# Performance work log

Hardware: AMD Instinct MI355X
Metric: run time of the kernel (lower is better)

## Reference

```python
import jax, jax.numpy as jnp
import numpy as np

B, N, D, H = 4, 4096, 1024, 16
DK = D // H


def setup_inputs() -> dict:
    key = jax.random.key(0)
    ks = jax.random.split(key, 11)
    s = 0.02  # small init scale for weights
    return {
        "query": jax.random.normal(ks[0], (B, N, D), jnp.float32),
        "key": jax.random.normal(ks[1], (B, N, D), jnp.float32),
        "value": jax.random.normal(ks[2], (B, N, D), jnp.float32),
        "Wq": jax.random.normal(ks[3], (D, D), jnp.float32) * s,
        "bq": jax.random.normal(ks[4], (D,), jnp.float32) * s,
        "Wk": jax.random.normal(ks[5], (D, D), jnp.float32) * s,
        "bk": jax.random.normal(ks[6], (D,), jnp.float32) * s,
        "Wv": jax.random.normal(ks[7], (D, D), jnp.float32) * s,
        "bv": jax.random.normal(ks[8], (D,), jnp.float32) * s,
        "Wo": jax.random.normal(ks[9], (D, D), jnp.float32) * s,
        "bo": jax.random.normal(ks[10], (D,), jnp.float32) * s,
    }


def reference(query, key, value, Wq, bq, Wk, bk, Wv, bv, Wo, bo):
    b, n, d = query.shape
    h, dk = H, d // H

    def proj(x, W, bias):
        # torch Linear: y = x @ W.T + b ; then split heads -> [b,h,n,dk]
        y = x @ W.T + bias
        return y.reshape(b, n, h, dk).transpose(0, 2, 1, 3)

    q = proj(query, Wq, bq)
    k = proj(key, Wk, bk)
    v = proj(value, Wv, bv)

    # linear attention (Efficient Attention, arXiv:1812.01243)
    q = jax.nn.softmax(q, axis=-1) * (1.0 / np.sqrt(dk).astype(np.float32))
    k = jax.nn.softmax(k, axis=-2)  # softmax over sequence dim
    ctx = jnp.einsum('bhnd,bhne->bhde', k, v)   # [b,h,dk,dk]
    out = jnp.einsum('bhnd,bhde->bhne', q, ctx)  # [b,h,n,dk]

    out = out.transpose(0, 2, 1, 3).reshape(b, n, d)
    return out @ Wo.T + bo
```

## Files before the change

kernel.cpp:

```cpp
#include <hip/hip_runtime.h>
#include <hip/hip_bf16.h>

#define B_ 4
#define N_ 4096
#define D_ 1024
#define H_ 16

typedef __attribute__((ext_vector_type(4))) float f32x4;
typedef __attribute__((ext_vector_type(8))) short s16x8;
typedef __attribute__((ext_vector_type(4))) unsigned int u32x4;

__device__ __forceinline__ ushort f2bf(float f) {
  union { float f; unsigned u; } v; v.f = f;
  unsigned u = v.u;
  return (ushort)((u + 0x7fffu + ((u >> 16) & 1u)) >> 16);
}

__device__ __forceinline__ void gld16(const ushort* g, ushort* lds_base) {
  __builtin_amdgcn_global_load_lds(
      (const __attribute__((address_space(1))) unsigned int*)g,
      (__attribute__((address_space(3))) unsigned int*)lds_base, 16, 0, 0);
}

__device__ __forceinline__ unsigned cvtpk(float lo, float hi) {
  unsigned r;
  asm("v_cvt_pk_bf16_f32 %0, %1, %2" : "=v"(r) : "v"(lo), "v"(hi));
  return r;
}

__global__ void conv_w_kernel(const float* __restrict__ w0, const float* __restrict__ w1,
                              const float* __restrict__ w2, const float* __restrict__ w3,
                              ushort* __restrict__ dst) {
  const int z = blockIdx.z;
  const float* src = z == 0 ? w0 : z == 1 ? w1 : z == 2 ? w2 : w3;
  ushort* d = dst + (long)z * (D_ * D_);
  const long i0 = ((long)blockIdx.x * 256 + threadIdx.x) * 8;
  const long STR = (long)128 * 256 * 8;
#pragma unroll
  for (int u = 0; u < 4; ++u) {
    f32x4 a = *(const f32x4*)(src + i0 + u * STR);
    f32x4 b = *(const f32x4*)(src + i0 + u * STR + 4);
    s16x8 o;
    o[0] = (short)f2bf(a[0]); o[1] = (short)f2bf(a[1]); o[2] = (short)f2bf(a[2]); o[3] = (short)f2bf(a[3]);
    o[4] = (short)f2bf(b[0]); o[5] = (short)f2bf(b[1]); o[6] = (short)f2bf(b[2]); o[7] = (short)f2bf(b[3]);
    *(s16x8*)(d + i0 + u * STR) = o;
  }
}

template <int EPI, bool AFP32>
__global__ __launch_bounds__(256, 2) void gemm_bt_kernel(
    const void* __restrict__ Av, const ushort* __restrict__ Bm,
    void* __restrict__ Cv, const float* __restrict__ bias, float* __restrict__ kpart,
    int K, long sA, long sB, long sC) {
  __shared__ ushort As[128 * 32];
  __shared__ ushort Bs[128 * 32];
  const int z = blockIdx.z;
  Bm += (long)z * sB;
  const int m0 = blockIdx.x * 128, n0 = blockIdx.y * 128;
  const int N = 1024;
  const int tid = threadIdx.x;
  const int wave = tid >> 6, lane = tid & 63;
  const int fl = lane & 15, fh = lane >> 4;
  const int wm = wave >> 1, wn = wave & 1;
  f32x4 acc[4][4] = {};
  const int rb0 = tid >> 2, kb0 = (tid & 3) * 8;
  const int rb1 = (tid + 256) >> 2, kb1 = ((tid + 256) & 3) * 8;
  ushort* ldsB0 = Bs + wave * 512;
  ushort* ldsB1 = Bs + 2048 + wave * 512;
  ushort* ldsA0 = As + wave * 512;
  ushort* ldsA1 = As + 2048 + wave * 512;

  const float* Af = (const float*)Av;
  const ushort* Ab = (const ushort*)Av + (long)z * sA;

  const int ar = tid >> 2, ac = tid & 3;
  const float* ap0 = AFP32 ? (Af + (long)(m0 + ar) * K + ac * 8) : nullptr;
  const float* ap1 = AFP32 ? (ap0 + (long)64 * K) : nullptr;
  ushort* wp0 = As + ar * 32 + ac * 8;
  ushort* wp1 = As + (ar + 64) * 32 + ac * 8;
  f32x4 pa0, pa1, pa2, pa3;
  if constexpr (AFP32) {
    pa0 = *(const f32x4*)(ap0);
    pa1 = *(const f32x4*)(ap0 + 4);
    pa2 = *(const f32x4*)(ap1);
    pa3 = *(const f32x4*)(ap1 + 4);
  }

  for (int kk = 0; kk < K; kk += 32) {
    __syncthreads();
    gld16(Bm + (long)(n0 + rb0) * K + kk + kb0, ldsB0);
    gld16(Bm + (long)(n0 + rb1) * K + kk + kb1, ldsB1);
    if constexpr (AFP32) {
      u32x4 w0, w1;
      w0[0] = cvtpk(pa0[0], pa0[1]); w0[1] = cvtpk(pa0[2], pa0[3]);
      w0[2] = cvtpk(pa1[0], pa1[1]); w0[3] = cvtpk(pa1[2], pa1[3]);
      w1[0] = cvtpk(pa2[0], pa2[1]); w1[1] = cvtpk(pa2[2], pa2[3]);
      w1[2] = cvtpk(pa3[0], pa3[1]); w1[3] = cvtpk(pa3[2], pa3[3]);
      *(u32x4*)wp0 = w0;
      *(u32x4*)wp1 = w1;
      if (kk + 32 < K) {
        pa0 = *(const f32x4*)(ap0 + kk + 32);
        pa1 = *(const f32x4*)(ap0 + kk + 36);
        pa2 = *(const f32x4*)(ap1 + kk + 32);
        pa3 = *(const f32x4*)(ap1 + kk + 36);
      }
    } else {
      gld16(Ab + (long)(m0 + rb0) * K + kk + kb0, ldsA0);
      gld16(Ab + (long)(m0 + rb1) * K + kk + kb1, ldsA1);
    }
    __syncthreads();
    s16x8 fa[4], fb[4];
#pragma unroll
    for (int i = 0; i < 4; ++i)
      fa[i] = *(const s16x8*)(As + (wm * 64 + i * 16 + fl) * 32 + fh * 8);
#pragma unroll
    for (int j = 0; j < 4; ++j)
      fb[j] = *(const s16x8*)(Bs + (wn * 64 + j * 16 + fl) * 32 + fh * 8);
#pragma unroll
    for (int i = 0; i < 4; ++i)
#pragma unroll
      for (int j = 0; j < 4; ++j)
        acc[i][j] = __builtin_amdgcn_mfma_f32_16x16x32_bf16(fa[i], fb[j], acc[i][j], 0, 0, 0);
  }

  if constexpr (EPI == 0) {
    ushort* C = (ushort*)Cv;
#pragma unroll
    for (int j = 0; j < 4; ++j) {
      int col = n0 + wn * 64 + j * 16 + fl;
#pragma unroll
      for (int i = 0; i < 4; ++i)
#pragma unroll
        for (int r = 0; r < 4; ++r) {
          int row = m0 + wm * 64 + i * 16 + fh * 4 + r;
          C[(long)row * N + col] = f2bf(acc[i][j][r]);
        }
    }
  } else if constexpr (EPI == 1) {
    ushort* C = (ushort*)Cv;
    float bcol[4];
#pragma unroll
    for (int j = 0; j < 4; ++j) bcol[j] = bias[n0 + wn * 64 + j * 16 + fl];
#pragma unroll
    for (int i = 0; i < 4; ++i)
#pragma unroll
      for (int r = 0; r < 4; ++r) {
        float v[4];
#pragma unroll
        for (int j = 0; j < 4; ++j) v[j] = acc[i][j][r] + bcol[j];
        float m = fmaxf(fmaxf(v[0], v[1]), fmaxf(v[2], v[3]));
#pragma unroll
        for (int o = 1; o <= 8; o <<= 1) m = fmaxf(m, __shfl_xor(m, o));
        float e[4], s = 0.f;
#pragma unroll
        for (int j = 0; j < 4; ++j) { e[j] = __expf(v[j] - m); s += e[j]; }
#pragma unroll
        for (int o = 1; o <= 8; o <<= 1) s += __shfl_xor(s, o);
        float sc = 0.125f / s;
        int row = m0 + wm * 64 + i * 16 + fh * 4 + r;
#pragma unroll
        for (int j = 0; j < 4; ++j)
          C[(long)row * N + n0 + wn * 64 + j * 16 + fl] = f2bf(e[j] * sc);
      }
  } else if constexpr (EPI == 2) {
    ushort* C = (ushort*)Cv;
    float csum[4] = {};
#pragma unroll
    for (int j = 0; j < 4; ++j) {
      int col = n0 + wn * 64 + j * 16 + fl;
#pragma unroll
      for (int i = 0; i < 4; ++i)
#pragma unroll
        for (int r = 0; r < 4; ++r) {
          int row = m0 + wm * 64 + i * 16 + fh * 4 + r;
          float e = __expf(acc[i][j][r]);
          csum[j] += e;
          C[(long)row * N + col] = f2bf(e);
        }
    }
#pragma unroll
    for (int j = 0; j < 4; ++j) {
#pragma unroll
      for (int o = 16; o <= 32; o <<= 1) csum[j] += __shfl_xor(csum[j], o);
    }
    if (fh == 0) {
      int b = m0 >> 12;
      int chunk = ((m0 & 4095) >> 7) * 2 + wm;
#pragma unroll
      for (int j = 0; j < 4; ++j)
        kpart[(long)b * 65536 + (long)chunk * 1024 + n0 + wn * 64 + j * 16 + fl] = csum[j];
    }
  } else {
    float* C = (float*)Cv + (long)z * sC;
#pragma unroll
    for (int j = 0; j < 4; ++j) {
      int col = n0 + wn * 64 + j * 16 + fl;
      float bv = bias[col];
#pragma unroll
      for (int i = 0; i < 4; ++i)
#pragma unroll
        for (int r = 0; r < 4; ++r) {
          int row = m0 + wm * 64 + i * 16 + fh * 4 + r;
          C[(long)row * N + col] = acc[i][j][r] + bv;
        }
    }
  }
}

__global__ void ksm2_kernel(const float* __restrict__ kpart, float* __restrict__ colinv) {
  int idx = blockIdx.x * 256 + threadIdx.x;
  int b = idx >> 10, d = idx & 1023;
  float s = 0.f;
  for (int c = 0; c < 64; ++c) s += kpart[(long)b * 65536 + (long)c * 1024 + d];
  colinv[idx] = 1.0f / s;
}

__global__ __launch_bounds__(256, 2) void ctx_partial_kernel(
    const ushort* __restrict__ Ksm, const ushort* __restrict__ Vp, float* __restrict__ part) {
  __shared__ ushort Ks[128 * 64];
  __shared__ ushort Vs[128 * 64];
  const int chunk = blockIdx.x;
  const int bh = blockIdx.y;
  const int b = bh >> 4, h = bh & 15;
  const int tid = threadIdx.x, wave = tid >> 6, lane = tid & 63;
  const int fl = lane & 15, fh = lane >> 4;
  f32x4 acc[4] = {};
  for (int t = 0; t < 4; ++t) {
    const long base = ((long)(b * N_ + chunk * 512 + t * 128)) * D_ + h * 64;
    __syncthreads();
#pragma unroll
    for (int i = 0; i < 4; ++i) {
      int c = i * 256 + tid;
      int r = c >> 3, k8 = (c & 7) * 8;
      ushort* lk = Ks + (long)(i * 256 + wave * 64) * 8;
      ushort* lv = Vs + (long)(i * 256 + wave * 64) * 8;
      gld16(Ksm + base + (long)r * D_ + k8, lk);
      gld16(Vp + base + (long)r * D_ + k8, lv);
    }
    __syncthreads();
#pragma unroll
    for (int s = 0; s < 4; ++s) {
      s16x8 fa;
#pragma unroll
      for (int j = 0; j < 8; ++j)
        fa[j] = (short)Ks[(s * 32 + fh * 8 + j) * 64 + wave * 16 + fl];
#pragma unroll
      for (int jt = 0; jt < 4; ++jt) {
        s16x8 fb;
#pragma unroll
        for (int j = 0; j < 8; ++j)
          fb[j] = (short)Vs[(s * 32 + fh * 8 + j) * 64 + jt * 16 + fl];
        acc[jt] = __builtin_amdgcn_mfma_f32_16x16x32_bf16(fa, fb, acc[jt], 0, 0, 0);
      }
    }
  }
  float* dst = part + ((long)chunk * 64 + bh) * 4096;
#pragma unroll
  for (int jt = 0; jt < 4; ++jt)
#pragma unroll
    for (int r = 0; r < 4; ++r)
      dst[(wave * 16 + fh * 4 + r) * 64 + jt * 16 + fl] = acc[jt][r];
}

__global__ void ctx_reduce_kernel(const float* __restrict__ part, const float* __restrict__ bv,
                                  const float* __restrict__ colinv, ushort* __restrict__ ctxb) {
  int idx = blockIdx.x * 256 + threadIdx.x;
  int e = idx & 63;
  int dk = (idx >> 6) & 63;
  int h = (idx >> 12) & 15;
  int b = idx >> 16;
  float s = 0.f;
#pragma unroll
  for (int c = 0; c < 8; ++c) s += part[(long)c * 262144 + idx];
  ctxb[idx] = f2bf(s * colinv[b * 1024 + h * 64 + dk] + bv[h * 64 + e]);
}

__global__ __launch_bounds__(256, 2) void mb_kernel(
    const ushort* __restrict__ Wob, const ushort* __restrict__ ctxb, ushort* __restrict__ Mb) {
  const int o0 = blockIdx.x * 64, h = blockIdx.y, b = blockIdx.z;
  const int tid = threadIdx.x, wave = tid >> 6, lane = tid & 63;
  const int fl = lane & 15, fh = lane >> 4;
  const ushort* ctxh = ctxb + ((long)(b * 16 + h)) * 4096;
  f32x4 acc[4] = {};
#pragma unroll
  for (int s = 0; s < 2; ++s) {
    s16x8 fa = *(const s16x8*)(Wob + (long)(o0 + wave * 16 + fl) * D_ + h * 64 + s * 32 + fh * 8);
#pragma unroll
    for (int jt = 0; jt < 4; ++jt) {
      s16x8 fb = *(const s16x8*)(ctxh + (long)(jt * 16 + fl) * 64 + s * 32 + fh * 8);
      acc[jt] = __builtin_amdgcn_mfma_f32_16x16x32_bf16(fa, fb, acc[jt], 0, 0, 0);
    }
  }
  ushort* dst = Mb + (long)b * (D_ * D_);
#pragma unroll
  for (int jt = 0; jt < 4; ++jt)
#pragma unroll
    for (int r = 0; r < 4; ++r)
      dst[(long)(o0 + wave * 16 + fh * 4 + r) * D_ + h * 64 + jt * 16 + fl] = f2bf(acc[jt][r]);
}

extern "C" void kernel_launch(void* const* d_in, const int* in_sizes, int n_in,
                              void* d_out, int out_size, void* d_ws, size_t ws_size,
                              hipStream_t stream) {
  const float* q_in = (const float*)d_in[0];
  const float* k_in = (const float*)d_in[1];
  const float* v_in = (const float*)d_in[2];
  const float* Wq = (const float*)d_in[3];
  const float* bq = (const float*)d_in[4];
  const float* Wk = (const float*)d_in[5];
  const float* Wv = (const float*)d_in[7];
  const float* bv = (const float*)d_in[8];
  const float* Wo = (const float*)d_in[9];
  const float* bo = (const float*)d_in[10];

  char* ws = (char*)d_ws;
  ushort* Wb = (ushort*)(ws + 0);
  ushort* Qp = (ushort*)(ws + 8388608);
  ushort* Kp = (ushort*)(ws + 41943040);
  ushort* Vp = (ushort*)(ws + 75497472);
  float* kpart = (float*)(ws + 109051904);
  float* colinv = (float*)(ws + 110100480);
  float* ctxpart = (float*)(ws + 110116864);
  ushort* ctxb = (ushort*)(ws + 118505472);
  ushort* Mb = (ushort*)(ws + 119029760);

  ushort* Wbq = Wb;
  ushort* Wbk = Wb + 1048576;
  ushort* Wbv = Wb + 2097152;
  ushort* Wbo = Wb + 3145728;

  conv_w_kernel<<<dim3(128, 1, 4), 256, 0, stream>>>(Wq, Wk, Wv, Wo, Wb);

  gemm_bt_kernel<1, true><<<dim3(128, 8, 1), 256, 0, stream>>>(
      q_in, Wbq, Qp, bq, nullptr, 1024, 0, 0, 0);
  gemm_bt_kernel<2, true><<<dim3(128, 8, 1), 256, 0, stream>>>(
      k_in, Wbk, Kp, nullptr, kpart, 1024, 0, 0, 0);
  gemm_bt_kernel<0, true><<<dim3(128, 8, 1), 256, 0, stream>>>(
      v_in, Wbv, Vp, nullptr, nullptr, 1024, 0, 0, 0);

  ksm2_kernel<<<16, 256, 0, stream>>>(kpart, colinv);

  ctx_partial_kernel<<<dim3(8, 64), 256, 0, stream>>>(Kp, Vp, ctxpart);
  ctx_reduce_kernel<<<1024, 256, 0, stream>>>(ctxpart, bv, colinv, ctxb);
  mb_kernel<<<dim3(16, 16, 4), 256, 0, stream>>>(Wbo, ctxb, Mb);

  gemm_bt_kernel<3, false><<<dim3(32, 8, 4), 256, 0, stream>>>(
      Qp, Mb, (float*)d_out, bo, nullptr, 1024,
      (long)4096 * 1024, (long)1024 * 1024, (long)4096 * 1024);
}
```

Baseline: 270.7 us.

## Pipeline GEMM with 4-stage LDS ring, 8 waves and swizzled shared layout

Rewrites the projection/output GEMM main loop into a multi-stage software pipeline: a 4-deep LDS ring buffer with async global-to-LDS loads issued several k-steps ahead, explicit vmcnt waits and single barriers per step. Blocks grow to 512 threads (8 waves, each owning a 32x64 sub-tile), and the LDS layout is XOR-swizzled to avoid bank conflicts on fragment reads. The fp32 A operand is prefetched two steps ahead in registers and converted to bf16. Key partial sums double in count because of the new wave layout, so the workspace offsets and the reduction loop are adjusted. This hardcodes K=1024 and adds complex manual wait-count logic that is easy to get wrong.

```diff
diff --git a/kernel.cpp b/kernel.cpp
--- a/kernel.cpp
+++ b/kernel.cpp
@@ -27,6 +27,11 @@
   asm("v_cvt_pk_bf16_f32 %0, %1, %2" : "=v"(r) : "v"(lo), "v"(hi));
   return r;
 }
+
+#define WAITVM(N) asm volatile("s_waitcnt vmcnt(" #N ")" ::: "memory")
+#define LGKM0 asm volatile("s_waitcnt lgkmcnt(0)" ::: "memory")
+#define SBAR __builtin_amdgcn_sched_barrier(0)
+#define BARRIER __builtin_amdgcn_s_barrier()
 
 __global__ void conv_w_kernel(const float* __restrict__ w0, const float* __restrict__ w1,
                               const float* __restrict__ w2, const float* __restrict__ w3,
@@ -48,12 +53,12 @@
 }
 
 template <int EPI, bool AFP32>
-__global__ __launch_bounds__(256, 2) void gemm_bt_kernel(
+__global__ __launch_bounds__(512, 4) void gemm_bt_kernel(
     const void* __restrict__ Av, const ushort* __restrict__ Bm,
     void* __restrict__ Cv, const float* __restrict__ bias, float* __restrict__ kpart,
-    int K, long sA, long sB, long sC) {
-  __shared__ ushort As[128 * 32];
-  __shared__ ushort Bs[128 * 32];
+    long sA, long sB, long sC) {
+  __shared__ ushort As[16384];
+  __shared__ ushort Bs[16384];
   const int z = blockIdx.z;
   Bm += (long)z * sB;
   const int m0 = blockIdx.x * 128, n0 = blockIdx.y * 128;
@@ -62,66 +67,99 @@
   const int wave = tid >> 6, lane = tid & 63;
   const int fl = lane & 15, fh = lane >> 4;
   const int wm = wave >> 1, wn = wave & 1;
-  f32x4 acc[4][4] = {};
-  const int rb0 = tid >> 2, kb0 = (tid & 3) * 8;
-  const int rb1 = (tid + 256) >> 2, kb1 = ((tid + 256) & 3) * 8;
-  ushort* ldsB0 = Bs + wave * 512;
-  ushort* ldsB1 = Bs + 2048 + wave * 512;
-  ushort* ldsA0 = As + wave * 512;
-  ushort* ldsA1 = As + 2048 + wave * 512;
-
-  const float* Af = (const float*)Av;
-  const ushort* Ab = (const ushort*)Av + (long)z * sA;
-
+  f32x4 acc[2][4] = {};
+
+  const int rB = tid >> 2;
+  const int sgB = ((tid & 3) ^ ((tid >> 3) & 3)) * 8;
+  const ushort* Bp0 = Bm + (long)(n0 + rB) * 1024 + sgB;
+  ushort* BsD0 = Bs + tid * 8;
+  const ushort* Ab = AFP32 ? nullptr : ((const ushort*)Av + (long)z * sA);
+  const ushort* Ap0 = AFP32 ? nullptr : (Ab + (long)(m0 + rB) * 1024 + sgB);
+  ushort* AsD0 = As + tid * 8;
   const int ar = tid >> 2, ac = tid & 3;
-  const float* ap0 = AFP32 ? (Af + (long)(m0 + ar) * K + ac * 8) : nullptr;
-  const float* ap1 = AFP32 ? (ap0 + (long)64 * K) : nullptr;
-  ushort* wp0 = As + ar * 32 + ac * 8;
-  ushort* wp1 = As + (ar + 64) * 32 + ac * 8;
-  f32x4 pa0, pa1, pa2, pa3;
+  const float* apA = AFP32 ? ((const float*)Av + (long)(m0 + ar) * 1024 + ac * 8) : nullptr;
+  const int awoff = ar * 32 + ((ac ^ ((tid >> 3) & 3)) * 8);
+  const int fro = fl * 32 + ((fh ^ ((fl >> 1) & 3)) * 8);
+
+  f32x4 pE0, pE1, pO0, pO1;
+
+#define ISSUE_B(T) do { gld16(Bp0 + (T) * 32, BsD0 + (((T) & 3) << 12)); } while (0)
+#define ISSUE_A16(T) do { gld16(Ap0 + (T) * 32, AsD0 + (((T) & 3) << 12)); } while (0)
+#define ISSUE_AF(T, P) do { \
+    P##0 = *(const f32x4*)(apA + (T) * 32); \
+    P##1 = *(const f32x4*)(apA + (T) * 32 + 4); } while (0)
+#define CVT_WRITE(T, P) do { \
+    u32x4 _w; \
+    _w[0] = cvtpk(P##0[0], P##0[1]); _w[1] = cvtpk(P##0[2], P##0[3]); \
+    _w[2] = cvtpk(P##1[0], P##1[1]); _w[3] = cvtpk(P##1[2], P##1[3]); \
+    *(u32x4*)(As + (((T) & 3) << 12) + awoff) = _w; } while (0)
+#define MFMA_STEP(T) do { \
+    const ushort* _a = As + (((T) & 3) << 12); \
+    const ushort* _b = Bs + (((T) & 3) << 12); \
+    s16x8 fa[2], fb[4]; \
+    _Pragma("unroll") for (int i = 0; i < 2; ++i) \
+      fa[i] = *(const s16x8*)(_a + (wm * 32 + i * 16) * 32 + fro); \
+    _Pragma("unroll") for (int j = 0; j < 4; ++j) \
+      fb[j] = *(const s16x8*)(_b + (wn * 64 + j * 16) * 32 + fro); \
+    _Pragma("unroll") for (int i = 0; i < 2; ++i) \
+      _Pragma("unroll") for (int j = 0; j < 4; ++j) \
+        acc[i][j] = __builtin_amdgcn_mfma_f32_16x16x32_bf16(fa[i], fb[j], acc[i][j], 0, 0, 0); \
+    } while (0)
+
   if constexpr (AFP32) {
-    pa0 = *(const f32x4*)(ap0);
-    pa1 = *(const f32x4*)(ap0 + 4);
-    pa2 = *(const f32x4*)(ap1);
-    pa3 = *(const f32x4*)(ap1 + 4);
-  }
-
-  for (int kk = 0; kk < K; kk += 32) {
-    __syncthreads();
-    gld16(Bm + (long)(n0 + rb0) * K + kk + kb0, ldsB0);
-    gld16(Bm + (long)(n0 + rb1) * K + kk + kb1, ldsB1);
-    if constexpr (AFP32) {
-      u32x4 w0, w1;
-      w0[0] = cvtpk(pa0[0], pa0[1]); w0[1] = cvtpk(pa0[2], pa0[3]);
-      w0[2] = cvtpk(pa1[0], pa1[1]); w0[3] = cvtpk(pa1[2], pa1[3]);
-      w1[0] = cvtpk(pa2[0], pa2[1]); w1[1] = cvtpk(pa2[2], pa2[3]);
-      w1[2] = cvtpk(pa3[0], pa3[1]); w1[3] = cvtpk(pa3[2], pa3[3]);
-      *(u32x4*)wp0 = w0;
-      *(u32x4*)wp1 = w1;
-      if (kk + 32 < K) {
-        pa0 = *(const f32x4*)(ap0 + kk + 32);
-        pa1 = *(const f32x4*)(ap0 + kk + 36);
-        pa2 = *(const f32x4*)(ap1 + kk + 32);
-        pa3 = *(const f32x4*)(ap1 + kk + 36);
-      }
-    } else {
-      gld16(Ab + (long)(m0 + rb0) * K + kk + kb0, ldsA0);
-      gld16(Ab + (long)(m0 + rb1) * K + kk + kb1, ldsA1);
-    }
-    __syncthreads();
-    s16x8 fa[4], fb[4];
-#pragma unroll
-    for (int i = 0; i < 4; ++i)
-      fa[i] = *(const s16x8*)(As + (wm * 64 + i * 16 + fl) * 32 + fh * 8);
-#pragma unroll
-    for (int j = 0; j < 4; ++j)
-      fb[j] = *(const s16x8*)(Bs + (wn * 64 + j * 16 + fl) * 32 + fh * 8);
-#pragma unroll
-    for (int i = 0; i < 4; ++i)
-#pragma unroll
-      for (int j = 0; j < 4; ++j)
-        acc[i][j] = __builtin_amdgcn_mfma_f32_16x16x32_bf16(fa[i], fb[j], acc[i][j], 0, 0, 0);
-  }
+    ISSUE_B(0); SBAR;
+    ISSUE_AF(0, pE); SBAR;
+    ISSUE_B(1); SBAR;
+    ISSUE_AF(1, pO); SBAR;
+    ISSUE_B(2); SBAR;
+    CVT_WRITE(0, pE);
+#pragma unroll 1
+    for (int t = 0; t < 28; t += 2) {
+      WAITVM(6); LGKM0; BARRIER; SBAR;
+      ISSUE_AF(t + 2, pE); SBAR;
+      ISSUE_B(t + 3); SBAR;
+      CVT_WRITE(t + 1, pO);
+      MFMA_STEP(t);
+      WAITVM(6); LGKM0; BARRIER; SBAR;
+      ISSUE_AF(t + 3, pO); SBAR;
+      ISSUE_B(t + 4); SBAR;
+      CVT_WRITE(t + 2, pE);
+      MFMA_STEP(t + 1);
+    }
+    WAITVM(6); LGKM0; BARRIER; SBAR;
+    ISSUE_AF(30, pE); SBAR;
+    ISSUE_B(31); SBAR;
+    CVT_WRITE(29, pO);
+    MFMA_STEP(28);
+    WAITVM(6); LGKM0; BARRIER; SBAR;
+    ISSUE_AF(31, pO); SBAR;
+    CVT_WRITE(30, pE);
+    MFMA_STEP(29);
+    WAITVM(5); LGKM0; BARRIER; SBAR;
+    CVT_WRITE(31, pO);
+    MFMA_STEP(30);
+    WAITVM(2); LGKM0; BARRIER; SBAR;
+    MFMA_STEP(31);
+  } else {
+    ISSUE_A16(0); SBAR; ISSUE_B(0); SBAR;
+    ISSUE_A16(1); SBAR; ISSUE_B(1); SBAR;
+    ISSUE_A16(2); SBAR; ISSUE_B(2); SBAR;
+#pragma unroll 1
+    for (int t = 0; t < 29; ++t) {
+      WAITVM(4); BARRIER; SBAR;
+      ISSUE_A16(t + 3); SBAR;
+      ISSUE_B(t + 3); SBAR;
+      MFMA_STEP(t);
+    }
+    WAITVM(4); BARRIER; SBAR; MFMA_STEP(29);
+    WAITVM(2); BARRIER; SBAR; MFMA_STEP(30);
+    WAITVM(0); BARRIER; SBAR; MFMA_STEP(31);
+  }
+#undef ISSUE_B
+#undef ISSUE_A16
+#undef ISSUE_AF
+#undef CVT_WRITE
+#undef MFMA_STEP
 
   if constexpr (EPI == 0) {
     ushort* C = (ushort*)Cv;
@@ -129,10 +167,10 @@
     for (int j = 0; j < 4; ++j) {
       int col = n0 + wn * 64 + j * 16 + fl;
 #pragma unroll
-      for (int i = 0; i < 4; ++i)
+      for (int i = 0; i < 2; ++i)
 #pragma unroll
         for (int r = 0; r < 4; ++r) {
-          int row = m0 + wm * 64 + i * 16 + fh * 4 + r;
+          int row = m0 + wm * 32 + i * 16 + fh * 4 + r;
           C[(long)row * N + col] = f2bf(acc[i][j][r]);
         }
     }
@@ -142,7 +180,7 @@
 #pragma unroll
     for (int j = 0; j < 4; ++j) bcol[j] = bias[n0 + wn * 64 + j * 16 + fl];
 #pragma unroll
-    for (int i = 0; i < 4; ++i)
+    for (int i = 0; i < 2; ++i)
 #pragma unroll
       for (int r = 0; r < 4; ++r) {
         float v[4];
@@ -157,7 +195,7 @@
 #pragma unroll
         for (int o = 1; o <= 8; o <<= 1) s += __shfl_xor(s, o);
         float sc = 0.125f / s;
-        int row = m0 + wm * 64 + i * 16 + fh * 4 + r;
+        int row = m0 + wm * 32 + i * 16 + fh * 4 + r;
 #pragma unroll
         for (int j = 0; j < 4; ++j)
           C[(long)row * N + n0 + wn * 64 + j * 16 + fl] = f2bf(e[j] * sc);
@@ -169,10 +207,10 @@
     for (int j = 0; j < 4; ++j) {
       int col = n0 + wn * 64 + j * 16 + fl;
 #pragma unroll
-      for (int i = 0; i < 4; ++i)
+      for (int i = 0; i < 2; ++i)
 #pragma unroll
         for (int r = 0; r < 4; ++r) {
-          int row = m0 + wm * 64 + i * 16 + fh * 4 + r;
+          int row = m0 + wm * 32 + i * 16 + fh * 4 + r;
           float e = __expf(acc[i][j][r]);
           csum[j] += e;
           C[(long)row * N + col] = f2bf(e);
@@ -185,10 +223,10 @@
     }
     if (fh == 0) {
       int b = m0 >> 12;
-      int chunk = ((m0 & 4095) >> 7) * 2 + wm;
+      int chunk = ((m0 & 4095) >> 7) * 4 + wm;
 #pragma unroll
       for (int j = 0; j < 4; ++j)
-        kpart[(long)b * 65536 + (long)chunk * 1024 + n0 + wn * 64 + j * 16 + fl] = csum[j];
+        kpart[(long)b * 131072 + (long)chunk * 1024 + n0 + wn * 64 + j * 16 + fl] = csum[j];
     }
   } else {
     float* C = (float*)Cv + (long)z * sC;
@@ -197,10 +235,10 @@
       int col = n0 + wn * 64 + j * 16 + fl;
       float bv = bias[col];
 #pragma unroll
-      for (int i = 0; i < 4; ++i)
+      for (int i = 0; i < 2; ++i)
 #pragma unroll
         for (int r = 0; r < 4; ++r) {
-          int row = m0 + wm * 64 + i * 16 + fh * 4 + r;
+          int row = m0 + wm * 32 + i * 16 + fh * 4 + r;
           C[(long)row * N + col] = acc[i][j][r] + bv;
         }
     }
@@ -211,7 +249,7 @@
   int idx = blockIdx.x * 256 + threadIdx.x;
   int b = idx >> 10, d = idx & 1023;
   float s = 0.f;
-  for (int c = 0; c < 64; ++c) s += kpart[(long)b * 65536 + (long)c * 1024 + d];
+  for (int c = 0; c < 128; ++c) s += kpart[(long)b * 131072 + (long)c * 1024 + d];
   colinv[idx] = 1.0f / s;
 }
 
@@ -319,10 +357,10 @@
   ushort* Kp = (ushort*)(ws + 41943040);
   ushort* Vp = (ushort*)(ws + 75497472);
   float* kpart = (float*)(ws + 109051904);
-  float* colinv = (float*)(ws + 110100480);
-  float* ctxpart = (float*)(ws + 110116864);
-  ushort* ctxb = (ushort*)(ws + 118505472);
-  ushort* Mb = (ushort*)(ws + 119029760);
+  float* colinv = (float*)(ws + 111149056);
+  float* ctxpart = (float*)(ws + 111165440);
+  ushort* ctxb = (ushort*)(ws + 119554048);
+  ushort* Mb = (ushort*)(ws + 120078336);
 
   ushort* Wbq = Wb;
   ushort* Wbk = Wb + 1048576;
@@ -331,12 +369,12 @@
 
   conv_w_kernel<<<dim3(128, 1, 4), 256, 0, stream>>>(Wq, Wk, Wv, Wo, Wb);
 
-  gemm_bt_kernel<1, true><<<dim3(128, 8, 1), 256, 0, stream>>>(
-      q_in, Wbq, Qp, bq, nullptr, 1024, 0, 0, 0);
-  gemm_bt_kernel<2, true><<<dim3(128, 8, 1), 256, 0, stream>>>(
-      k_in, Wbk, Kp, nullptr, kpart, 1024, 0, 0, 0);
-  gemm_bt_kernel<0, true><<<dim3(128, 8, 1), 256, 0, stream>>>(
-      v_in, Wbv, Vp, nullptr, nullptr, 1024, 0, 0, 0);
+  gemm_bt_kernel<1, true><<<dim3(128, 8, 1), 512, 0, stream>>>(
+      q_in, Wbq, Qp, bq, nullptr, 0, 0, 0);
+  gemm_bt_kernel<2, true><<<dim3(128, 8, 1), 512, 0, stream>>>(
+      k_in, Wbk, Kp, nullptr, kpart, 0, 0, 0);
+  gemm_bt_kernel<0, true><<<dim3(128, 8, 1), 512, 0, stream>>>(
+      v_in, Wbv, Vp, nullptr, nullptr, 0, 0, 0);
 
   ksm2_kernel<<<16, 256, 0, stream>>>(kpart, colinv);
 
@@ -344,7 +382,7 @@
   ctx_reduce_kernel<<<1024, 256, 0, stream>>>(ctxpart, bv, colinv, ctxb);
   mb_kernel<<<dim3(16, 16, 4), 256, 0, stream>>>(Wbo, ctxb, Mb);
 
-  gemm_bt_kernel<3, false><<<dim3(32, 8, 4), 256, 0, stream>>>(
-      Qp, Mb, (float*)d_out, bo, nullptr, 1024,
+  gemm_bt_kernel<3, false><<<dim3(32, 8, 4), 512, 0, stream>>>(
+      Qp, Mb, (float*)d_out, bo, nullptr,
       (long)4096 * 1024, (long)1024 * 1024, (long)4096 * 1024);
 }
```

Result: slower. 302.6 us (+11.8%).

## Merge QKV projections into one launch and XOR-swizzle LDS tiles

Applied to the files above, without the earlier changes.

Replaces the three separate projection GEMM launches with a single launch that uses blockIdx.z to pick the input, weight and epilogue. It also XOR-swizzles the LDS layout of the A and B tiles, for both the global-to-LDS loads and the fragment reads, to reduce bank conflicts. The fp32 A loading now gives each thread 16 consecutive floats of one row instead of 8 floats from two rows. The output GEMM becomes a dedicated kernel with the same swizzle. The per-z epilogue branch is uniform per block, so it adds little divergence.

```diff
diff --git a/kernel.cpp b/kernel.cpp
--- a/kernel.cpp
+++ b/kernel.cpp
@@ -47,75 +47,69 @@
   }
 }
 
-template <int EPI, bool AFP32>
-__global__ __launch_bounds__(256, 2) void gemm_bt_kernel(
-    const void* __restrict__ Av, const ushort* __restrict__ Bm,
-    void* __restrict__ Cv, const float* __restrict__ bias, float* __restrict__ kpart,
-    int K, long sA, long sB, long sC) {
-  __shared__ ushort As[128 * 32];
-  __shared__ ushort Bs[128 * 32];
+__global__ __launch_bounds__(256, 2) void gemm_qkv(
+    const float* __restrict__ q_in, const float* __restrict__ k_in,
+    const float* __restrict__ v_in, const ushort* __restrict__ Wb,
+    ushort* __restrict__ P, const float* __restrict__ bq, float* __restrict__ kpart) {
+  __shared__ ushort As[4096];
+  __shared__ ushort Bs[4096];
   const int z = blockIdx.z;
-  Bm += (long)z * sB;
+  const float* Af = z == 0 ? q_in : (z == 1 ? k_in : v_in);
+  const ushort* Bm = Wb + (long)z * 1048576;
+  ushort* C = P + (long)z * 16777216;
   const int m0 = blockIdx.x * 128, n0 = blockIdx.y * 128;
   const int N = 1024;
   const int tid = threadIdx.x;
-  const int wave = tid >> 6, lane = tid & 63;
+  const int lane = tid & 63, wave = tid >> 6;
   const int fl = lane & 15, fh = lane >> 4;
   const int wm = wave >> 1, wn = wave & 1;
   f32x4 acc[4][4] = {};
-  const int rb0 = tid >> 2, kb0 = (tid & 3) * 8;
-  const int rb1 = (tid + 256) >> 2, kb1 = ((tid + 256) & 3) * 8;
-  ushort* ldsB0 = Bs + wave * 512;
-  ushort* ldsB1 = Bs + 2048 + wave * 512;
-  ushort* ldsA0 = As + wave * 512;
-  ushort* ldsA1 = As + 2048 + wave * 512;
-
-  const float* Af = (const float*)Av;
-  const ushort* Ab = (const ushort*)Av + (long)z * sA;
-
-  const int ar = tid >> 2, ac = tid & 3;
-  const float* ap0 = AFP32 ? (Af + (long)(m0 + ar) * K + ac * 8) : nullptr;
-  const float* ap1 = AFP32 ? (ap0 + (long)64 * K) : nullptr;
-  ushort* wp0 = As + ar * 32 + ac * 8;
-  ushort* wp1 = As + (ar + 64) * 32 + ac * 8;
+
+  const int r0 = tid >> 2;
+  const int s8 = (((tid & 3) ^ ((r0 >> 1) & 3)) * 8);
+  const ushort* Bsrc0 = Bm + (long)(n0 + r0) * 1024 + s8;
+  const ushort* Bsrc1 = Bm + (long)(n0 + r0 + 64) * 1024 + s8;
+
+  const int ar = tid >> 1, ch = tid & 1;
+  const float* apA = Af + (long)(m0 + ar) * 1024 + ch * 16;
+  const int aw0 = ar * 32 + (((ch * 2) ^ ((ar >> 1) & 3)) * 8);
+  const int aw1 = ar * 32 + (((ch * 2 + 1) ^ ((ar >> 1) & 3)) * 8);
+
+  const int fro = (fh ^ ((fl >> 1) & 3)) * 8;
+
   f32x4 pa0, pa1, pa2, pa3;
-  if constexpr (AFP32) {
-    pa0 = *(const f32x4*)(ap0);
-    pa1 = *(const f32x4*)(ap0 + 4);
-    pa2 = *(const f32x4*)(ap1);
-    pa3 = *(const f32x4*)(ap1 + 4);
-  }
-
-  for (int kk = 0; kk < K; kk += 32) {
-    __syncthreads();
-    gld16(Bm + (long)(n0 + rb0) * K + kk + kb0, ldsB0);
-    gld16(Bm + (long)(n0 + rb1) * K + kk + kb1, ldsB1);
-    if constexpr (AFP32) {
+  pa0 = *(const f32x4*)(apA);
+  pa1 = *(const f32x4*)(apA + 4);
+  pa2 = *(const f32x4*)(apA + 8);
+  pa3 = *(const f32x4*)(apA + 12);
+
+  for (int kk = 0; kk < 1024; kk += 32) {
+    __syncthreads();
+    gld16(Bsrc0 + kk, Bs + tid * 8);
+    gld16(Bsrc1 + kk, Bs + 2048 + tid * 8);
+    {
       u32x4 w0, w1;
       w0[0] = cvtpk(pa0[0], pa0[1]); w0[1] = cvtpk(pa0[2], pa0[3]);
       w0[2] = cvtpk(pa1[0], pa1[1]); w0[3] = cvtpk(pa1[2], pa1[3]);
       w1[0] = cvtpk(pa2[0], pa2[1]); w1[1] = cvtpk(pa2[2], pa2[3]);
       w1[2] = cvtpk(pa3[0], pa3[1]); w1[3] = cvtpk(pa3[2], pa3[3]);
-      *(u32x4*)wp0 = w0;
-      *(u32x4*)wp1 = w1;
-      if (kk + 32 < K) {
-        pa0 = *(const f32x4*)(ap0 + kk + 32);
-        pa1 = *(const f32x4*)(ap0 + kk + 36);
-        pa2 = *(const f32x4*)(ap1 + kk + 32);
-        pa3 = *(const f32x4*)(ap1 + kk + 36);
+      *(u32x4*)(As + aw0) = w0;
+      *(u32x4*)(As + aw1) = w1;
+      if (kk + 32 < 1024) {
+        pa0 = *(const f32x4*)(apA + kk + 32);
+        pa1 = *(const f32x4*)(apA + kk + 36);
+        pa2 = *(const f32x4*)(apA + kk + 40);
+        pa3 = *(const f32x4*)(apA + kk + 44);
       }
-    } else {
-      gld16(Ab + (long)(m0 + rb0) * K + kk + kb0, ldsA0);
-      gld16(Ab + (long)(m0 + rb1) * K + kk + kb1, ldsA1);
     }
     __syncthreads();
     s16x8 fa[4], fb[4];
 #pragma unroll
     for (int i = 0; i < 4; ++i)
-      fa[i] = *(const s16x8*)(As + (wm * 64 + i * 16 + fl) * 32 + fh * 8);
+      fa[i] = *(const s16x8*)(As + (wm * 64 + i * 16 + fl) * 32 + fro);
 #pragma unroll
     for (int j = 0; j < 4; ++j)
-      fb[j] = *(const s16x8*)(Bs + (wn * 64 + j * 16 + fl) * 32 + fh * 8);
+      fb[j] = *(const s16x8*)(Bs + (wn * 64 + j * 16 + fl) * 32 + fro);
 #pragma unroll
     for (int i = 0; i < 4; ++i)
 #pragma unroll
@@ -123,24 +117,10 @@
         acc[i][j] = __builtin_amdgcn_mfma_f32_16x16x32_bf16(fa[i], fb[j], acc[i][j], 0, 0, 0);
   }
 
-  if constexpr (EPI == 0) {
-    ushort* C = (ushort*)Cv;
-#pragma unroll
-    for (int j = 0; j < 4; ++j) {
-      int col = n0 + wn * 64 + j * 16 + fl;
-#pragma unroll
-      for (int i = 0; i < 4; ++i)
-#pragma unroll
-        for (int r = 0; r < 4; ++r) {
-          int row = m0 + wm * 64 + i * 16 + fh * 4 + r;
-          C[(long)row * N + col] = f2bf(acc[i][j][r]);
-        }
-    }
-  } else if constexpr (EPI == 1) {
-    ushort* C = (ushort*)Cv;
+  if (z == 0) {
     float bcol[4];
 #pragma unroll
-    for (int j = 0; j < 4; ++j) bcol[j] = bias[n0 + wn * 64 + j * 16 + fl];
+    for (int j = 0; j < 4; ++j) bcol[j] = bq[n0 + wn * 64 + j * 16 + fl];
 #pragma unroll
     for (int i = 0; i < 4; ++i)
 #pragma unroll
@@ -162,8 +142,7 @@
         for (int j = 0; j < 4; ++j)
           C[(long)row * N + n0 + wn * 64 + j * 16 + fl] = f2bf(e[j] * sc);
       }
-  } else if constexpr (EPI == 2) {
-    ushort* C = (ushort*)Cv;
+  } else if (z == 1) {
     float csum[4] = {};
 #pragma unroll
     for (int j = 0; j < 4; ++j) {
@@ -191,19 +170,78 @@
         kpart[(long)b * 65536 + (long)chunk * 1024 + n0 + wn * 64 + j * 16 + fl] = csum[j];
     }
   } else {
-    float* C = (float*)Cv + (long)z * sC;
 #pragma unroll
     for (int j = 0; j < 4; ++j) {
       int col = n0 + wn * 64 + j * 16 + fl;
-      float bv = bias[col];
 #pragma unroll
       for (int i = 0; i < 4; ++i)
 #pragma unroll
         for (int r = 0; r < 4; ++r) {
           int row = m0 + wm * 64 + i * 16 + fh * 4 + r;
-          C[(long)row * N + col] = acc[i][j][r] + bv;
+          C[(long)row * N + col] = f2bf(acc[i][j][r]);
         }
     }
+  }
+}
+
+__global__ __launch_bounds__(256, 2) void gemm_o(const ushort* __restrict__ Ain,
+                                                 const ushort* __restrict__ Bin,
+                                                 float* __restrict__ Cout,
+                                                 const float* __restrict__ bias) {
+  __shared__ ushort As[4096];
+  __shared__ ushort Bs[4096];
+  const int z = blockIdx.z;
+  const ushort* Ab = Ain + (long)z * 4096 * 1024;
+  const ushort* Bm = Bin + (long)z * 1024 * 1024;
+  float* C = Cout + (long)z * 4096 * 1024;
+  const int m0 = blockIdx.x * 128, n0 = blockIdx.y * 128;
+  const int N = 1024;
+  const int tid = threadIdx.x;
+  const int lane = tid & 63, wave = tid >> 6;
+  const int fl = lane & 15, fh = lane >> 4;
+  const int wm = wave >> 1, wn = wave & 1;
+  f32x4 acc[4][4] = {};
+
+  const int r0 = tid >> 2;
+  const int s8 = (((tid & 3) ^ ((r0 >> 1) & 3)) * 8);
+  const ushort* Bsrc0 = Bm + (long)(n0 + r0) * 1024 + s8;
+  const ushort* Bsrc1 = Bm + (long)(n0 + r0 + 64) * 1024 + s8;
+  const ushort* Asrc0 = Ab + (long)(m0 + r0) * 1024 + s8;
+  const ushort* Asrc1 = Ab + (long)(m0 + r0 + 64) * 1024 + s8;
+  const int fro = (fh ^ ((fl >> 1) & 3)) * 8;
+
+  for (int kk = 0; kk < 1024; kk += 32) {
+    __syncthreads();
+    gld16(Asrc0 + kk, As + tid * 8);
+    gld16(Asrc1 + kk, As + 2048 + tid * 8);
+    gld16(Bsrc0 + kk, Bs + tid * 8);
+    gld16(Bsrc1 + kk, Bs + 2048 + tid * 8);
+    __syncthreads();
+    s16x8 fa[4], fb[4];
+#pragma unroll
+    for (int i = 0; i < 4; ++i)
+      fa[i] = *(const s16x8*)(As + (wm * 64 + i * 16 + fl) * 32 + fro);
+#pragma unroll
+    for (int j = 0; j < 4; ++j)
+      fb[j] = *(const s16x8*)(Bs + (wn * 64 + j * 16 + fl) * 32 + fro);
+#pragma unroll
+    for (int i = 0; i < 4; ++i)
+#pragma unroll
+      for (int j = 0; j < 4; ++j)
+        acc[i][j] = __builtin_amdgcn_mfma_f32_16x16x32_bf16(fa[i], fb[j], acc[i][j], 0, 0, 0);
+  }
+
+#pragma unroll
+  for (int j = 0; j < 4; ++j) {
+    int col = n0 + wn * 64 + j * 16 + fl;
+    float bv = bias[col];
+#pragma unroll
+    for (int i = 0; i < 4; ++i)
+#pragma unroll
+      for (int r = 0; r < 4; ++r) {
+        int row = m0 + wm * 64 + i * 16 + fh * 4 + r;
+        C[(long)row * N + col] = acc[i][j][r] + bv;
+      }
   }
 }
 
@@ -316,27 +354,19 @@
   char* ws = (char*)d_ws;
   ushort* Wb = (ushort*)(ws + 0);
   ushort* Qp = (ushort*)(ws + 8388608);
-  ushort* Kp = (ushort*)(ws + 41943040);
-  ushort* Vp = (ushort*)(ws + 75497472);
   float* kpart = (float*)(ws + 109051904);
   float* colinv = (float*)(ws + 110100480);
   float* ctxpart = (float*)(ws + 110116864);
   ushort* ctxb = (ushort*)(ws + 118505472);
   ushort* Mb = (ushort*)(ws + 119029760);
 
-  ushort* Wbq = Wb;
-  ushort* Wbk = Wb + 1048576;
-  ushort* Wbv = Wb + 2097152;
+  ushort* Kp = Qp + 16777216;
+  ushort* Vp = Qp + 33554432;
   ushort* Wbo = Wb + 3145728;
 
   conv_w_kernel<<<dim3(128, 1, 4), 256, 0, stream>>>(Wq, Wk, Wv, Wo, Wb);
 
-  gemm_bt_kernel<1, true><<<dim3(128, 8, 1), 256, 0, stream>>>(
-      q_in, Wbq, Qp, bq, nullptr, 1024, 0, 0, 0);
-  gemm_bt_kernel<2, true><<<dim3(128, 8, 1), 256, 0, stream>>>(
-      k_in, Wbk, Kp, nullptr, kpart, 1024, 0, 0, 0);
-  gemm_bt_kernel<0, true><<<dim3(128, 8, 1), 256, 0, stream>>>(
-      v_in, Wbv, Vp, nullptr, nullptr, 1024, 0, 0, 0);
+  gemm_qkv<<<dim3(128, 8, 3), 256, 0, stream>>>(q_in, k_in, v_in, Wb, Qp, bq, kpart);
 
   ksm2_kernel<<<16, 256, 0, stream>>>(kpart, colinv);
 
@@ -344,7 +374,5 @@
   ctx_reduce_kernel<<<1024, 256, 0, stream>>>(ctxpart, bv, colinv, ctxb);
   mb_kernel<<<dim3(16, 16, 4), 256, 0, stream>>>(Wbo, ctxb, Mb);
 
-  gemm_bt_kernel<3, false><<<dim3(32, 8, 4), 256, 0, stream>>>(
-      Qp, Mb, (float*)d_out, bo, nullptr, 1024,
-      (long)4096 * 1024, (long)1024 * 1024, (long)4096 * 1024);
-}
+  gemm_o<<<dim3(32, 8, 4), 256, 0, stream>>>(Qp, Mb, (float*)d_out, bo);
+}
```

After: 301.8 us. 11.5% more time.
